# Kernel tuning notes

Measured on AMD Instinct MI355X. Metric: run time of the kernel, lower is better.

## Reference

```python
import jax, jax.numpy as jnp
import numpy as np

D_IN = 1024
D_OUT = 1024
NUM_HEADS = 16
HEAD_DIM = D_OUT // NUM_HEADS


def setup_inputs() -> dict:
    key = jax.random.key(0)
    kx, kq, kk, kv = jax.random.split(key, 4)
    x = jax.random.normal(kx, (2, 2048, D_IN), dtype=jnp.float32)
    W_q = jax.random.normal(kq, (D_IN, D_OUT), dtype=jnp.float32)
    W_k = jax.random.normal(kk, (D_IN, D_OUT), dtype=jnp.float32)
    W_v = jax.random.normal(kv, (D_IN, D_OUT), dtype=jnp.float32)
    return {"x": x, "W_q": W_q, "W_k": W_k, "W_v": W_v}


def reference(x, W_q, W_k, W_v):
    B, S, _ = x.shape
    H, Dh = NUM_HEADS, HEAD_DIM
    # project and split heads -> [B, H, S, Dh]
    q = (x @ W_q).reshape(B, S, H, Dh).transpose(0, 2, 1, 3)
    k = (x @ W_k).reshape(B, S, H, Dh).transpose(0, 2, 1, 3)
    v = (x @ W_v).reshape(B, S, H, Dh).transpose(0, 2, 1, 3)
    scores = jnp.einsum('bhqd,bhkd->bhqk', q, k) / jnp.sqrt(jnp.float32(Dh))
    causal = jnp.tril(jnp.ones((S, S), dtype=bool))  # True where allowed
    scores = jnp.where(causal[None, None], scores, -jnp.inf)
    weights = jax.nn.softmax(scores, axis=-1)
    ctx = jnp.einsum('bhqk,bhkd->bhqd', weights, v)
    return ctx.transpose(0, 2, 1, 3).reshape(B, S, H * Dh)
```

## Files before the change

### kernel.cpp

```cpp
#include <hip/hip_runtime.h>
#include <hip/hip_bf16.h>

#define B 2
#define S 2048
#define DIN 1024
#define DOUT 1024
#define NH 16
#define DH 64
#define M_TOT (B * S)

typedef __attribute__((ext_vector_type(8))) short bf16x8;
typedef __attribute__((ext_vector_type(8))) unsigned short u16x8;
typedef __attribute__((ext_vector_type(4))) float f32x4;
typedef __attribute__((ext_vector_type(16))) float f32x16;

#define ASTRIDE 4194304
#define WSTRIDE 1048576

__device__ __forceinline__ ushort f2bf(float x) {
    union { float f; unsigned u; } c; c.f = x;
    unsigned r = (c.u + 0x7FFFu + ((c.u >> 16) & 1u)) >> 16;
    return (ushort)r;
}
__device__ __forceinline__ float bf2f(ushort h) {
    union { unsigned u; float f; } c; c.u = ((unsigned)h) << 16;
    return c.f;
}
__device__ __forceinline__ f32x4 mfma16(bf16x8 a, bf16x8 b, f32x4 c) {
    return __builtin_amdgcn_mfma_f32_16x16x32_bf16(a, b, c, 0, 0, 0);
}
__device__ __forceinline__ f32x16 mfma32(bf16x8 a, bf16x8 b, f32x16 c) {
    return __builtin_amdgcn_mfma_f32_32x32x16_bf16(a, b, c, 0, 0, 0);
}
__device__ __forceinline__ unsigned cvt_pk(float lo, float hi) {
    unsigned r;
    asm("v_cvt_pk_bf16_f32 %0, %1, %2" : "=v"(r) : "v"(lo), "v"(hi));
    return r;
}
__device__ __forceinline__ float exp2fast(float x) {
    float r;
    asm("v_exp_f32 %0, %1" : "=v"(r) : "v"(x));
    return r;
}


__global__ __launch_bounds__(256) void split_x(const float* __restrict__ x,
                                               ushort* __restrict__ xs) {
    const size_t gid = (size_t)blockIdx.x * 256 + threadIdx.x;
    const float4 v = *reinterpret_cast<const float4*>(x + gid * 4);
    const float in[4] = {v.x, v.y, v.z, v.w};
    ushort h0[4], h1[4];
#pragma unroll
    for (int e = 0; e < 4; ++e) {
        h0[e] = f2bf(in[e]);
        h1[e] = f2bf(in[e] - bf2f(h0[e]));
    }
    const size_t o = gid * 4;
    *reinterpret_cast<ushort4*>(xs + o)           = ushort4{h0[0], h0[1], h0[2], h0[3]};
    *reinterpret_cast<ushort4*>(xs + ASTRIDE + o) = ushort4{h1[0], h1[1], h1[2], h1[3]};
}

__global__ __launch_bounds__(256) void split_wT3(const float* __restrict__ W0,
                                                 const float* __restrict__ W1,
                                                 const float* __restrict__ W2,
                                                 ushort* __restrict__ wt) {
    __shared__ float Ws[64][68];
    const int tid = threadIdx.x;
    const int k0 = blockIdx.x << 6;
    const int n0 = blockIdx.y << 6;
    const int wi = blockIdx.z;
    const float* W = (wi == 0) ? W0 : (wi == 1) ? W1 : W2;
    ushort* wto = wt + (size_t)wi * 2 * WSTRIDE;

    const int r = tid >> 2;
    const int cb = (tid & 3) << 2;
#pragma unroll
    for (int it = 0; it < 4; ++it) {
        const int c = cb + (it << 4);
        *reinterpret_cast<float4*>(&Ws[r][c]) =
            *reinterpret_cast<const float4*>(&W[(size_t)(k0 + r) * 1024 + n0 + c]);
    }
    __syncthreads();
    const int rn = tid >> 2;
    const int kc = (tid & 3) << 4;
    u16x8 o0[2], o1[2];
#pragma unroll
    for (int half = 0; half < 2; ++half)
#pragma unroll
        for (int i = 0; i < 8; ++i) {
            const float x = Ws[kc + (half << 3) + i][rn];
            const ushort a = f2bf(x);
            o0[half][i] = a;
            o1[half][i] = f2bf(x - bf2f(a));
        }
    const size_t base = (size_t)(n0 + rn) * 1024 + k0 + kc;
    *reinterpret_cast<u16x8*>(wto + base)               = o0[0];
    *reinterpret_cast<u16x8*>(wto + base + 8)           = o0[1];
    *reinterpret_cast<u16x8*>(wto + WSTRIDE + base)     = o1[0];
    *reinterpret_cast<u16x8*>(wto + WSTRIDE + base + 8) = o1[1];
}

__global__ __launch_bounds__(256, 2) void proj_fused3(const ushort* __restrict__ xsp,
                                                      const ushort* __restrict__ wtsp,
                                                      float* __restrict__ qf,
                                                      ushort* __restrict__ ksp,
                                                      ushort* __restrict__ vtsp) {
    __shared__ __align__(16) ushort SL[36864];

    const int tid = threadIdx.x;
    const int lane = tid & 63;
    const int w = tid >> 6;
    const int swz = (blockIdx.x & 7) * 64 + (blockIdx.x >> 3);
    const int n0 = (swz & 15) << 6;
    const int m0 = (swz >> 4) << 7;
    const int col = lane & 15;
    const int glane = lane >> 4;
    const int lrow = lane >> 3;
    const int sl8 = ((lane & 7) ^ lrow) << 3;

    f32x4 accq[2][4], acck[2][4], accv[2][4];
#pragma unroll
    for (int mi = 0; mi < 2; ++mi)
#pragma unroll
        for (int nj = 0; nj < 4; ++nj) {
            accq[mi][nj] = f32x4{0.f, 0.f, 0.f, 0.f};
            acck[mi][nj] = f32x4{0.f, 0.f, 0.f, 0.f};
            accv[mi][nj] = f32x4{0.f, 0.f, 0.f, 0.f};
        }

    for (int k0 = 0; k0 < DIN; k0 += 64) {
        __syncthreads();
#pragma unroll
        for (int i = 0; i < 18; ++i) {
            const int u = (i << 2) | w;
            const ushort* g;
            if (u < 32) {
                const int sp = u >> 4, rb = u & 15;
                g = xsp + (size_t)sp * ASTRIDE + (size_t)(m0 + (rb << 3) + lrow) * 1024 + k0 + sl8;
            } else {
                const int v = u - 32;
                const int bi = v >> 3;
                const int rb = v & 7;
                g = wtsp + (size_t)bi * WSTRIDE + (size_t)(n0 + (rb << 3) + lrow) * 1024 + k0 + sl8;
            }
            __builtin_amdgcn_global_load_lds(g, &SL[u * 512], 16, 0, 0);
        }
        __syncthreads();

#pragma unroll
        for (int st = 0; st < 2; ++st) {
            const int sw = (((st << 2) | glane) ^ (col & 7)) << 3;
            bf16x8 a[2][2];
#pragma unroll
            for (int sp = 0; sp < 2; ++sp)
#pragma unroll
                for (int mi = 0; mi < 2; ++mi) {
                    const int arow = (w << 5) + (mi << 4) + col;
                    a[sp][mi] = *reinterpret_cast<const bf16x8*>(&SL[sp * 8192 + arow * 64 + sw]);
                }
#pragma unroll
            for (int nj = 0; nj < 4; ++nj) {
                const int brow = (nj << 4) + col;
                const int bb = 16384 + brow * 64 + sw;
                const bf16x8 bq0 = *reinterpret_cast<const bf16x8*>(&SL[bb]);
                const bf16x8 bq1 = *reinterpret_cast<const bf16x8*>(&SL[bb + 4096]);
                const bf16x8 bk0 = *reinterpret_cast<const bf16x8*>(&SL[bb + 8192]);
                const bf16x8 bk1 = *reinterpret_cast<const bf16x8*>(&SL[bb + 12288]);
                const bf16x8 bv0 = *reinterpret_cast<const bf16x8*>(&SL[bb + 16384]);
#pragma unroll
                for (int mi = 0; mi < 2; ++mi) {
                    accq[mi][nj] = mfma16(a[0][mi], bq0, accq[mi][nj]);
                    accq[mi][nj] = mfma16(a[1][mi], bq0, accq[mi][nj]);
                    accq[mi][nj] = mfma16(a[0][mi], bq1, accq[mi][nj]);
                    accq[mi][nj] = mfma16(a[1][mi], bq1, accq[mi][nj]);
                    acck[mi][nj] = mfma16(a[0][mi], bk0, acck[mi][nj]);
                    acck[mi][nj] = mfma16(a[1][mi], bk0, acck[mi][nj]);
                    acck[mi][nj] = mfma16(a[0][mi], bk1, acck[mi][nj]);
                    acck[mi][nj] = mfma16(a[1][mi], bk1, acck[mi][nj]);
                    accv[mi][nj] = mfma16(a[0][mi], bv0, accv[mi][nj]);
                    accv[mi][nj] = mfma16(a[1][mi], bv0, accv[mi][nj]);
                }
            }
        }
    }

    const int b = m0 >> 11;
    const int h = n0 >> 6;
    const size_t bh_off = (size_t)(b * NH + h) * S * DH;
#pragma unroll
    for (int mi = 0; mi < 2; ++mi)
#pragma unroll
        for (int r = 0; r < 4; ++r) {
            const int srow = (m0 & (S - 1)) + (w << 5) + (mi << 4) + (glane << 2) + r;
#pragma unroll
            for (int nj = 0; nj < 4; ++nj) {
                const size_t o = bh_off + (size_t)srow * DH + (nj << 4) + col;
                qf[o] = accq[mi][nj][r];
                const float xk = acck[mi][nj][r];
                const ushort k0s = f2bf(xk);
                ksp[o] = k0s;
                ksp[ASTRIDE + o] = f2bf(xk - bf2f(k0s));
            }
        }

    float* SLf = reinterpret_cast<float*>(SL);
    __syncthreads();
#pragma unroll
    for (int mi = 0; mi < 2; ++mi)
#pragma unroll
        for (int r = 0; r < 4; ++r) {
            const int sl_ = (w << 5) + (mi << 4) + (glane << 2) + r;
#pragma unroll
            for (int nj = 0; nj < 4; ++nj)
                SLf[((nj << 4) + col) * 132 + sl_] = accv[mi][nj][r];
        }
    __syncthreads();
    {
        const int d = tid >> 2;
        const size_t vb = ((size_t)(b * NH + h) * DH + d) * S + (m0 & (S - 1));
#pragma unroll
        for (int blk = 0; blk < 2; ++blk) {
            const int sb = ((tid & 3) << 5) + (blk << 4);
            u16x8 oA, oB;
#pragma unroll
            for (int i = 0; i < 8; ++i) {
                const int jA = (i < 4) ? i : i + 4;
                const int jB = (i < 4) ? i + 4 : i + 8;
                oA[i] = f2bf(SLf[d * 132 + sb + jA]);
                oB[i] = f2bf(SLf[d * 132 + sb + jB]);
            }
            *reinterpret_cast<u16x8*>(vtsp + vb + sb)     = oA;
            *reinterpret_cast<u16x8*>(vtsp + vb + sb + 8) = oB;
        }
    }
}

__global__ __launch_bounds__(256, 2) void attn_mfma7(const float* __restrict__ Qf,
                                                     const ushort* __restrict__ ksp,
                                                     const ushort* __restrict__ vtsp,
                                                     float* __restrict__ out) {
    __shared__ __align__(16) ushort SB[2][12288];

    const int tid = threadIdx.x;
    const int lane = tid & 63;
    const int w = tid >> 6;

    const int xcd = blockIdx.x & 7;
    const int u_ = blockIdx.x >> 3;
    int bh, qt;
    if (u_ < 32) { bh = (xcd << 2) | (u_ >> 4);                 qt = 15 - (u_ & 15); }
    else         { const int v2 = u_ - 32; bh = (xcd << 2) | 2 | (v2 >> 4); qt = v2 & 15; }

    const int q0 = qt << 7;
    const int qw0 = q0 + (w << 5);
    const int hi = lane >> 5;
    const int ql = lane & 31;
    const int qg = qw0 + ql;
    const int lrow = lane >> 3;
    const int sl8 = ((lane & 7) ^ lrow) << 3;

    bf16x8 qb[3][4];
    {
        const float* qp = Qf + ((size_t)bh * S + qg) * DH + (hi << 3);
#pragma unroll
        for (int dc = 0; dc < 4; ++dc) {
            const float4 f0 = *reinterpret_cast<const float4*>(qp + (dc << 4));
            const float4 f1 = *reinterpret_cast<const float4*>(qp + (dc << 4) + 4);
            const float xs[8] = {f0.x, f0.y, f0.z, f0.w, f1.x, f1.y, f1.z, f1.w};
#pragma unroll
            for (int e = 0; e < 8; ++e) {
                const float x = xs[e] * 0.18033688011112042f;
                const ushort h0 = f2bf(x);
                const float r1 = x - bf2f(h0);
                const ushort h1 = f2bf(r1);
                qb[0][dc][e] = (short)h0;
                qb[1][dc][e] = (short)h1;
                qb[2][dc][e] = (short)f2bf(r1 - bf2f(h1));
            }
        }
    }

    f32x16 O[2];
#pragma unroll
    for (int ds = 0; ds < 2; ++ds)
#pragma unroll
        for (int r = 0; r < 16; ++r) O[ds][r] = 0.f;
    float m_ = -INFINITY, l_ = 0.f;

    const size_t kbase = (size_t)bh * S * DH;
    const size_t vbase = (size_t)bh * DH * S;

#define ISSUE_KV(K0, BUF)                                                               \
    {                                                                                   \
        _Pragma("unroll")                                                               \
        for (int i = 0; i < 6; ++i) {                                                   \
            const int u = (i << 2) | w;                                                 \
            const ushort* gp;                                                           \
            if (u < 16) {                                                               \
                const int sp = u >> 3, rb = u & 7;                                      \
                gp = ksp + (size_t)sp * ASTRIDE + kbase +                               \
                     (size_t)((K0) + (rb << 3) + lrow) * DH + sl8;                      \
            } else {                                                                    \
                const int rb = u & 7;                                                   \
                gp = vtsp + vbase + (size_t)((rb << 3) + lrow) * S + (K0) + sl8;        \
            }                                                                           \
            __builtin_amdgcn_global_load_lds(gp, &SB[BUF][u * 512], 16, 0, 0);          \
        }                                                                               \
    }

    ISSUE_KV(0, 0);
    __syncthreads();

    const int ktmax = (q0 >> 6) + 1;
    for (int kt = 0; kt <= ktmax; ++kt) {
        const int k0 = kt << 6;
        const int cur = kt & 1;
        if (kt < ktmax) ISSUE_KV(k0 + 64, cur ^ 1);

        const bool active = (k0 <= qw0 + 31);
        if (active) {
            const ushort* KL = &SB[cur][0];
            const ushort* VL = &SB[cur][8192];

            f32x16 Sf[2];
#pragma unroll
            for (int ks = 0; ks < 2; ++ks)
#pragma unroll
                for (int r = 0; r < 16; ++r) Sf[ks][r] = 0.f;
#pragma unroll
            for (int ks = 0; ks < 2; ++ks) {
#pragma unroll
                for (int dc = 0; dc < 4; ++dc) {
                    const int row = (ks << 5) + ql;
                    const int eo = row * 64 + ((((dc << 1) | hi) ^ (row & 7)) << 3);
                    const bf16x8 ka = *reinterpret_cast<const bf16x8*>(&KL[eo]);
                    const bf16x8 kb = *reinterpret_cast<const bf16x8*>(&KL[4096 + eo]);
                    Sf[ks] = mfma32(ka, qb[0][dc], Sf[ks]);
                    Sf[ks] = mfma32(ka, qb[1][dc], Sf[ks]);
                    Sf[ks] = mfma32(ka, qb[2][dc], Sf[ks]);
                    Sf[ks] = mfma32(kb, qb[0][dc], Sf[ks]);
                    Sf[ks] = mfma32(kb, qb[1][dc], Sf[ks]);
                }
            }

            if (k0 + 63 > qw0) {
#pragma unroll
                for (int ks = 0; ks < 2; ++ks)
#pragma unroll
                    for (int r = 0; r < 16; ++r) {
                        const int kg = k0 + (ks << 5) + (r & 3) + ((r >> 2) << 3) + (hi << 2);
                        if (kg > qg) Sf[ks][r] = -1e30f;
                    }
            }

            float mx[8];
#pragma unroll
            for (int i = 0; i < 8; ++i)
                mx[i] = fmaxf(fmaxf(Sf[0][i], Sf[0][i + 8]),
                              fmaxf(Sf[1][i], Sf[1][i + 8]));
            float rm = fmaxf(fmaxf(fmaxf(mx[0], mx[1]), fmaxf(mx[2], mx[3])),
                             fmaxf(fmaxf(mx[4], mx[5]), fmaxf(mx[6], mx[7])));
            rm = fmaxf(rm, __shfl_xor(rm, 32));
            if (__any(rm > m_ + 8.f)) {
                const float nm = fmaxf(m_, rm);
                const float sc = exp2fast(m_ - nm);
                m_ = nm;
                l_ *= sc;
#pragma unroll
                for (int ds = 0; ds < 2; ++ds)
#pragma unroll
                    for (int r = 0; r < 16; ++r) O[ds][r] *= sc;
            }

            float rsa[4] = {0.f, 0.f, 0.f, 0.f};
            bf16x8 pb[4];
#pragma unroll
            for (int ks = 0; ks < 2; ++ks) {
                float p[16];
#pragma unroll
                for (int r = 0; r < 16; ++r) {
                    p[r] = exp2fast(Sf[ks][r] - m_);
                    rsa[r & 3] += p[r];
                }
#pragma unroll
                for (int c = 0; c < 2; ++c) {
                    union { unsigned u[4]; bf16x8 v; } pw;
                    pw.u[0] = cvt_pk(p[(c << 3) + 0], p[(c << 3) + 1]);
                    pw.u[1] = cvt_pk(p[(c << 3) + 2], p[(c << 3) + 3]);
                    pw.u[2] = cvt_pk(p[(c << 3) + 4], p[(c << 3) + 5]);
                    pw.u[3] = cvt_pk(p[(c << 3) + 6], p[(c << 3) + 7]);
                    pb[(ks << 1) + c] = pw.v;
                }
            }
            float rs = (rsa[0] + rsa[1]) + (rsa[2] + rsa[3]);
            rs += __shfl_xor(rs, 32);
            l_ += rs;

#pragma unroll
            for (int ds = 0; ds < 2; ++ds)
#pragma unroll
                for (int kc = 0; kc < 4; ++kc) {
                    const int row = (ds << 5) + ql;
                    const int eo = row * 64 + ((((kc << 1) | hi) ^ (row & 7)) << 3);
                    const bf16x8 va = *reinterpret_cast<const bf16x8*>(&VL[eo]);
                    O[ds] = mfma32(va, pb[kc], O[ds]);
                }
        }
        __syncthreads();
    }

    const float inv = 1.f / l_;
    const int b = bh >> 4, h = bh & (NH - 1);
    float* op = out + ((size_t)(b * S + qg)) * DOUT + h * DH;
#pragma unroll
    for (int ds = 0; ds < 2; ++ds)
#pragma unroll
        for (int rg = 0; rg < 4; ++rg) {
            float4 v;
            v.x = O[ds][(rg << 2) + 0] * inv;
            v.y = O[ds][(rg << 2) + 1] * inv;
            v.z = O[ds][(rg << 2) + 2] * inv;
            v.w = O[ds][(rg << 2) + 3] * inv;
            *reinterpret_cast<float4*>(&op[(ds << 5) + (rg << 3) + (hi << 2)]) = v;
        }
#undef ISSUE_KV
}

__global__ __launch_bounds__(256) void proj_f32(const float* __restrict__ A,
                                                const float* __restrict__ W,
                                                float* __restrict__ outf) {
    __shared__ float As[16][68];
    __shared__ float Bs[16][68];
    const int tid = threadIdx.x;
    const int m0 = blockIdx.x * 64;
    const int n0 = blockIdx.y * 64;
    const int tm = tid >> 4, tn = tid & 15;
    const int la_r = tid >> 2, la_c = (tid & 3) << 2;
    const int lb_r = tid >> 4, lb_c = (tid & 15) << 2;

    float acc[4][4];
#pragma unroll
    for (int i = 0; i < 4; ++i)
#pragma unroll
        for (int j = 0; j < 4; ++j) acc[i][j] = 0.f;

    for (int k0 = 0; k0 < DIN; k0 += 16) {
        const float4 av = *reinterpret_cast<const float4*>(&A[(size_t)(m0 + la_r) * DIN + k0 + la_c]);
        const float4 bv = *reinterpret_cast<const float4*>(&W[(size_t)(k0 + lb_r) * DOUT + n0 + lb_c]);
        __syncthreads();
        As[la_c + 0][la_r] = av.x; As[la_c + 1][la_r] = av.y;
        As[la_c + 2][la_r] = av.z; As[la_c + 3][la_r] = av.w;
        *reinterpret_cast<float4*>(&Bs[lb_r][lb_c]) = bv;
        __syncthreads();
#pragma unroll
        for (int kk = 0; kk < 16; ++kk) {
            const float4 a = *reinterpret_cast<const float4*>(&As[kk][tm << 2]);
            const float4 b = *reinterpret_cast<const float4*>(&Bs[kk][tn << 2]);
            const float aa[4] = {a.x, a.y, a.z, a.w};
            const float bb[4] = {b.x, b.y, b.z, b.w};
#pragma unroll
            for (int i = 0; i < 4; ++i)
#pragma unroll
                for (int j = 0; j < 4; ++j) acc[i][j] += aa[i] * bb[j];
        }
    }
    const int b = m0 >> 11;
    const int s_base = (m0 & (S - 1)) + (tm << 2);
    const int h = n0 >> 6;
    const int dh = tn << 2;
    float* obase = outf + ((size_t)(b * NH + h) * S) * DH;
#pragma unroll
    for (int i = 0; i < 4; ++i) {
        float4 v;
        v.x = acc[i][0]; v.y = acc[i][1]; v.z = acc[i][2]; v.w = acc[i][3];
        *reinterpret_cast<float4*>(&obase[(size_t)(s_base + i) * DH + dh]) = v;
    }
}

__global__ __launch_bounds__(256) void attn_f32(const float* __restrict__ Q,
                                                const float* __restrict__ K,
                                                const float* __restrict__ V,
                                                float* __restrict__ out) {
    __shared__ float Qs[64][68];
    __shared__ float Ks[64][68];
    __shared__ float Vs[64][68];
    __shared__ float Ps[64][68];
    const int tid = threadIdx.x;
    const int bh = blockIdx.x & 31;
    const int qt = 31 - (blockIdx.x >> 5);
    const int q0 = qt << 6;
    const int tq = tid >> 4, tk = tid & 15;
    const int sr = tid >> 2, sc = (tid & 3) << 2;

    const float* qbase = Q + ((size_t)bh * S + q0) * DH;
    const float* kbase = K + (size_t)bh * S * DH;
    const float* vbase = V + (size_t)bh * S * DH;
#pragma unroll
    for (int it = 0; it < 4; ++it) {
        const int d0 = sc + (it << 4);
        const float4 v = *reinterpret_cast<const float4*>(&qbase[(size_t)sr * DH + d0]);
        Qs[d0 + 0][sr] = v.x; Qs[d0 + 1][sr] = v.y;
        Qs[d0 + 2][sr] = v.z; Qs[d0 + 3][sr] = v.w;
    }
    float C[4][4];
#pragma unroll
    for (int i = 0; i < 4; ++i)
#pragma unroll
        for (int j = 0; j < 4; ++j) C[i][j] = 0.f;
    float m[4] = {-1e30f, -1e30f, -1e30f, -1e30f};
    float l[4] = {0.f, 0.f, 0.f, 0.f};

    for (int kt = 0; kt <= qt; ++kt) {
        const int k0 = kt << 6;
        float4 kv[4], vv[4];
#pragma unroll
        for (int it = 0; it < 4; ++it) {
            const int d0 = sc + (it << 4);
            kv[it] = *reinterpret_cast<const float4*>(&kbase[(size_t)(k0 + sr) * DH + d0]);
            vv[it] = *reinterpret_cast<const float4*>(&vbase[(size_t)(k0 + sr) * DH + d0]);
        }
        __syncthreads();
#pragma unroll
        for (int it = 0; it < 4; ++it) {
            const int d0 = sc + (it << 4);
            Ks[d0 + 0][sr] = kv[it].x; Ks[d0 + 1][sr] = kv[it].y;
            Ks[d0 + 2][sr] = kv[it].z; Ks[d0 + 3][sr] = kv[it].w;
            *reinterpret_cast<float4*>(&Vs[sr][d0]) = vv[it];
        }
        __syncthreads();

        float s[4][4];
#pragma unroll
        for (int i = 0; i < 4; ++i)
#pragma unroll
            for (int j = 0; j < 4; ++j) s[i][j] = 0.f;
#pragma unroll 16
        for (int d = 0; d < 64; ++d) {
            const float4 qf4 = *reinterpret_cast<const float4*>(&Qs[d][tq << 2]);
            const float4 kf4 = *reinterpret_cast<const float4*>(&Ks[d][tk << 2]);
            const float qa[4] = {qf4.x, qf4.y, qf4.z, qf4.w};
            const float ka[4] = {kf4.x, kf4.y, kf4.z, kf4.w};
#pragma unroll
            for (int i = 0; i < 4; ++i)
#pragma unroll
                for (int j = 0; j < 4; ++j) s[i][j] += qa[i] * ka[j];
        }
        if (kt == qt) {
#pragma unroll
            for (int i = 0; i < 4; ++i) {
                const int qg = q0 + (tq << 2) + i;
#pragma unroll
                for (int j = 0; j < 4; ++j) {
                    const int kg = k0 + (tk << 2) + j;
                    s[i][j] = (kg <= qg) ? s[i][j] * 0.125f : -1e30f;
                }
            }
        } else {
#pragma unroll
            for (int i = 0; i < 4; ++i)
#pragma unroll
                for (int j = 0; j < 4; ++j) s[i][j] *= 0.125f;
        }
#pragma unroll
        for (int i = 0; i < 4; ++i) {
            float rm = fmaxf(fmaxf(s[i][0], s[i][1]), fmaxf(s[i][2], s[i][3]));
#pragma unroll
            for (int off = 1; off < 16; off <<= 1) rm = fmaxf(rm, __shfl_xor(rm, off));
            const float mn = fmaxf(m[i], rm);
            const float scale = __expf(m[i] - mn);
            float rs = 0.f;
#pragma unroll
            for (int j = 0; j < 4; ++j) {
                s[i][j] = __expf(s[i][j] - mn);
                rs += s[i][j];
            }
#pragma unroll
            for (int off = 1; off < 16; off <<= 1) rs += __shfl_xor(rs, off);
            l[i] = l[i] * scale + rs;
            m[i] = mn;
#pragma unroll
            for (int j = 0; j < 4; ++j) C[i][j] *= scale;
            *reinterpret_cast<float4*>(&Ps[(tq << 2) + i][tk << 2]) =
                make_float4(s[i][0], s[i][1], s[i][2], s[i][3]);
        }
        __syncthreads();
#pragma unroll 4
        for (int kc = 0; kc < 16; ++kc) {
            float4 pf[4], vf[4];
#pragma unroll
            for (int i = 0; i < 4; ++i)
                pf[i] = *reinterpret_cast<const float4*>(&Ps[(tq << 2) + i][kc << 2]);
#pragma unroll
            for (int j = 0; j < 4; ++j)
                vf[j] = *reinterpret_cast<const float4*>(&Vs[(kc << 2) + j][tk << 2]);
#pragma unroll
            for (int i = 0; i < 4; ++i) {
                const float pa[4] = {pf[i].x, pf[i].y, pf[i].z, pf[i].w};
#pragma unroll
                for (int j = 0; j < 4; ++j) {
                    C[i][j] += pa[0] * ((const float*)&vf[0])[j]
                             + pa[1] * ((const float*)&vf[1])[j]
                             + pa[2] * ((const float*)&vf[2])[j]
                             + pa[3] * ((const float*)&vf[3])[j];
                }
            }
        }
        __syncthreads();
    }
    const int b = bh >> 4, h = bh & (NH - 1);
#pragma unroll
    for (int i = 0; i < 4; ++i) {
        const int qg = q0 + (tq << 2) + i;
        const float inv = 1.f / l[i];
        float4 v;
        v.x = C[i][0] * inv; v.y = C[i][1] * inv;
        v.z = C[i][2] * inv; v.w = C[i][3] * inv;
        *reinterpret_cast<float4*>(&out[((size_t)(b * S + qg)) * DOUT + h * DH + (tk << 2)]) = v;
    }
}

extern "C" void kernel_launch(void* const* d_in, const int* in_sizes, int n_in,
                              void* d_out, int out_size, void* d_ws, size_t ws_size,
                              hipStream_t stream) {
    const float* x  = (const float*)d_in[0];
    const float* Wq = (const float*)d_in[1];
    const float* Wk = (const float*)d_in[2];
    const float* Wv = (const float*)d_in[3];
    float* out = (float*)d_out;

    char* ws = (char*)d_ws;
    const size_t MB = 1024 * 1024;

    if (ws_size >= 68 * MB) {
        ushort* wtsp = (ushort*)(ws);
        ushort* xsp  = (ushort*)(ws + 12 * MB);
        float*  qf   = (float*)(ws + 28 * MB);
        ushort* ksp  = (ushort*)(ws + 44 * MB);
        ushort* vtsp = (ushort*)(ws + 60 * MB);

        split_x<<<4096, 256, 0, stream>>>(x, xsp);
        split_wT3<<<dim3(16, 16, 3), 256, 0, stream>>>(Wq, Wk, Wv, wtsp);
        proj_fused3<<<512, 256, 0, stream>>>(xsp, wtsp, qf, ksp, vtsp);
        attn_mfma7<<<512, 256, 0, stream>>>(qf, ksp, vtsp, out);
    } else {
        float* qws = (float*)d_ws;
        float* kws = qws + (size_t)M_TOT * DOUT;
        float* vws = kws + (size_t)M_TOT * DOUT;
        dim3 pgrid(M_TOT / 64, DOUT / 64);
        proj_f32<<<pgrid, 256, 0, stream>>>(x, Wq, qws);
        proj_f32<<<pgrid, 256, 0, stream>>>(x, Wk, kws);
        proj_f32<<<pgrid, 256, 0, stream>>>(x, Wv, vws);
        attn_f32<<<32 * 32, 256, 0, stream>>>(qws, kws, vws, out);
    }
}
```

Before: 144.5 us.

## Double-buffer projection LDS tiles, drop lo*lo MFMA terms, transpose V via MFMA operand swap

The fused QKV projection now double-buffers its shared-memory tiles, issuing the next K-slice's global-to-LDS loads before computing on the current one, so each step needs one barrier instead of two. It also drops the lo*lo correction MFMAs in the split-bf16 products, which lowers precision slightly. V is computed with swapped MFMA operands so the accumulator comes out already transposed and is stored directly, removing the LDS transpose pass. LDS use doubles to about 144KB per block, which may cut occupancy from two blocks per CU to one.

```diff
diff --git a/kernel.cpp b/kernel.cpp
--- a/kernel.cpp
+++ b/kernel.cpp
@@ -100,12 +100,12 @@
     *reinterpret_cast<u16x8*>(wto + WSTRIDE + base + 8) = o1[1];
 }
 
-__global__ __launch_bounds__(256, 2) void proj_fused3(const ushort* __restrict__ xsp,
-                                                      const ushort* __restrict__ wtsp,
-                                                      float* __restrict__ qf,
-                                                      ushort* __restrict__ ksp,
-                                                      ushort* __restrict__ vtsp) {
-    __shared__ __align__(16) ushort SL[36864];
+__global__ __launch_bounds__(256) void proj_fused4(const ushort* __restrict__ xsp,
+                                                   const ushort* __restrict__ wtsp,
+                                                   float* __restrict__ qf,
+                                                   ushort* __restrict__ ksp,
+                                                   ushort* __restrict__ vtsp) {
+    __shared__ __align__(16) ushort SB[2][36864];
 
     const int tid = threadIdx.x;
     const int lane = tid & 63;
@@ -128,25 +128,35 @@
             accv[mi][nj] = f32x4{0.f, 0.f, 0.f, 0.f};
         }
 
-    for (int k0 = 0; k0 < DIN; k0 += 64) {
-        __syncthreads();
-#pragma unroll
-        for (int i = 0; i < 18; ++i) {
-            const int u = (i << 2) | w;
-            const ushort* g;
-            if (u < 32) {
-                const int sp = u >> 4, rb = u & 15;
-                g = xsp + (size_t)sp * ASTRIDE + (size_t)(m0 + (rb << 3) + lrow) * 1024 + k0 + sl8;
-            } else {
-                const int v = u - 32;
-                const int bi = v >> 3;
-                const int rb = v & 7;
-                g = wtsp + (size_t)bi * WSTRIDE + (size_t)(n0 + (rb << 3) + lrow) * 1024 + k0 + sl8;
-            }
-            __builtin_amdgcn_global_load_lds(g, &SL[u * 512], 16, 0, 0);
-        }
-        __syncthreads();
-
+#define PISSUE(K0, BUF)                                                                 \
+    {                                                                                   \
+        _Pragma("unroll")                                                               \
+        for (int i = 0; i < 18; ++i) {                                                  \
+            const int u = (i << 2) | w;                                                 \
+            const ushort* g;                                                            \
+            if (u < 32) {                                                               \
+                const int sp = u >> 4, rb = u & 15;                                     \
+                g = xsp + (size_t)sp * ASTRIDE +                                        \
+                    (size_t)(m0 + (rb << 3) + lrow) * 1024 + (K0) + sl8;                \
+            } else {                                                                    \
+                const int v = u - 32;                                                   \
+                const int bi = v >> 3;                  \
+                const int rb = v & 7;                                                   \
+                g = wtsp + (size_t)bi * WSTRIDE +                                       \
+                    (size_t)(n0 + (rb << 3) + lrow) * 1024 + (K0) + sl8;                \
+            }                                                                           \
+            __builtin_amdgcn_global_load_lds(g, &SB[BUF][u * 512], 16, 0, 0);           \
+        }                                                                               \
+    }
+
+    PISSUE(0, 0);
+    __syncthreads();
+
+    for (int kt = 0; kt < 16; ++kt) {
+        const int cur = kt & 1;
+        if (kt < 15) PISSUE((kt + 1) << 6, cur ^ 1);
+
+        const ushort* SL = SB[cur];
 #pragma unroll
         for (int st = 0; st < 2; ++st) {
             const int sw = (((st << 2) | glane) ^ (col & 7)) << 3;
@@ -172,17 +182,17 @@
                     accq[mi][nj] = mfma16(a[0][mi], bq0, accq[mi][nj]);
                     accq[mi][nj] = mfma16(a[1][mi], bq0, accq[mi][nj]);
                     accq[mi][nj] = mfma16(a[0][mi], bq1, accq[mi][nj]);
-                    accq[mi][nj] = mfma16(a[1][mi], bq1, accq[mi][nj]);
                     acck[mi][nj] = mfma16(a[0][mi], bk0, acck[mi][nj]);
                     acck[mi][nj] = mfma16(a[1][mi], bk0, acck[mi][nj]);
                     acck[mi][nj] = mfma16(a[0][mi], bk1, acck[mi][nj]);
-                    acck[mi][nj] = mfma16(a[1][mi], bk1, acck[mi][nj]);
-                    accv[mi][nj] = mfma16(a[0][mi], bv0, accv[mi][nj]);
-                    accv[mi][nj] = mfma16(a[1][mi], bv0, accv[mi][nj]);
-                }
-            }
-        }
-    }
+                    accv[mi][nj] = mfma16(bv0, a[0][mi], accv[mi][nj]);
+                    accv[mi][nj] = mfma16(bv0, a[1][mi], accv[mi][nj]);
+                }
+            }
+        }
+        __syncthreads();
+    }
+#undef PISSUE
 
     const int b = m0 >> 11;
     const int h = n0 >> 6;
@@ -203,35 +213,19 @@
             }
         }
 
-    float* SLf = reinterpret_cast<float*>(SL);
-    __syncthreads();
-#pragma unroll
-    for (int mi = 0; mi < 2; ++mi)
-#pragma unroll
-        for (int r = 0; r < 4; ++r) {
-            const int sl_ = (w << 5) + (mi << 4) + (glane << 2) + r;
-#pragma unroll
-            for (int nj = 0; nj < 4; ++nj)
-                SLf[((nj << 4) + col) * 132 + sl_] = accv[mi][nj][r];
-        }
-    __syncthreads();
-    {
-        const int d = tid >> 2;
-        const size_t vb = ((size_t)(b * NH + h) * DH + d) * S + (m0 & (S - 1));
-#pragma unroll
-        for (int blk = 0; blk < 2; ++blk) {
-            const int sb = ((tid & 3) << 5) + (blk << 4);
-            u16x8 oA, oB;
-#pragma unroll
-            for (int i = 0; i < 8; ++i) {
-                const int jA = (i < 4) ? i : i + 4;
-                const int jB = (i < 4) ? i + 4 : i + 8;
-                oA[i] = f2bf(SLf[d * 132 + sb + jA]);
-                oB[i] = f2bf(SLf[d * 132 + sb + jB]);
-            }
-            *reinterpret_cast<u16x8*>(vtsp + vb + sb)     = oA;
-            *reinterpret_cast<u16x8*>(vtsp + vb + sb + 8) = oB;
-        }
+    const int cm = col >> 2;
+    const int colp = (col & 3) | ((((cm & 1) << 1) | (cm >> 1)) << 2);
+    const size_t vbh = (size_t)(b * NH + h) * DH * S;
+#pragma unroll
+    for (int mi = 0; mi < 2; ++mi) {
+        const int s = (m0 & (S - 1)) + (w << 5) + (mi << 4) + colp;
+#pragma unroll
+        for (int nj = 0; nj < 4; ++nj)
+#pragma unroll
+            for (int r = 0; r < 4; ++r) {
+                const int d = (nj << 4) + (glane << 2) + r;
+                vtsp[vbh + (size_t)d * S + s] = f2bf(accv[mi][nj][r]);
+            }
     }
 }
 
@@ -640,7 +634,7 @@
 
         split_x<<<4096, 256, 0, stream>>>(x, xsp);
         split_wT3<<<dim3(16, 16, 3), 256, 0, stream>>>(Wq, Wk, Wv, wtsp);
-        proj_fused3<<<512, 256, 0, stream>>>(xsp, wtsp, qf, ksp, vtsp);
+        proj_fused4<<<512, 256, 0, stream>>>(xsp, wtsp, qf, ksp, vtsp);
         attn_mfma7<<<512, 256, 0, stream>>>(qf, ksp, vtsp, out);
     } else {
         float* qws = (float*)d_ws;
```

Measured after the change: 143.4 us. No clear change (-0.7%).

## Drop lo*lo split-bf16 MFMAs and write V transposed directly from registers

Applied to the files above, without the earlier changes.

Removes the lo×lo correction MFMA from the Q and K split-bf16 products, cutting one of four MFMAs per term. V now uses hi×hi plus lo-x×hi-W only. The V MFMA operands are swapped so the accumulator comes out transposed, which lets V^T be stored straight from registers with a permuted column index. That replaces the shared-memory transpose and its two barriers. The trade is a small loss of precision and narrower, less coalesced 2-byte scattered stores for V^T.

```diff
diff --git a/kernel.cpp b/kernel.cpp
--- a/kernel.cpp
+++ b/kernel.cpp
@@ -100,7 +100,7 @@
     *reinterpret_cast<u16x8*>(wto + WSTRIDE + base + 8) = o1[1];
 }
 
-__global__ __launch_bounds__(256, 2) void proj_fused3(const ushort* __restrict__ xsp,
+__global__ __launch_bounds__(256, 2) void proj_fused5(const ushort* __restrict__ xsp,
                                                       const ushort* __restrict__ wtsp,
                                                       float* __restrict__ qf,
                                                       ushort* __restrict__ ksp,
@@ -172,13 +172,11 @@
                     accq[mi][nj] = mfma16(a[0][mi], bq0, accq[mi][nj]);
                     accq[mi][nj] = mfma16(a[1][mi], bq0, accq[mi][nj]);
                     accq[mi][nj] = mfma16(a[0][mi], bq1, accq[mi][nj]);
-                    accq[mi][nj] = mfma16(a[1][mi], bq1, accq[mi][nj]);
                     acck[mi][nj] = mfma16(a[0][mi], bk0, acck[mi][nj]);
                     acck[mi][nj] = mfma16(a[1][mi], bk0, acck[mi][nj]);
                     acck[mi][nj] = mfma16(a[0][mi], bk1, acck[mi][nj]);
-                    acck[mi][nj] = mfma16(a[1][mi], bk1, acck[mi][nj]);
-                    accv[mi][nj] = mfma16(a[0][mi], bv0, accv[mi][nj]);
-                    accv[mi][nj] = mfma16(a[1][mi], bv0, accv[mi][nj]);
+                    accv[mi][nj] = mfma16(bv0, a[0][mi], accv[mi][nj]);
+                    accv[mi][nj] = mfma16(bv0, a[1][mi], accv[mi][nj]);
                 }
             }
         }
@@ -203,35 +201,19 @@
             }
         }
 
-    float* SLf = reinterpret_cast<float*>(SL);
-    __syncthreads();
-#pragma unroll
-    for (int mi = 0; mi < 2; ++mi)
-#pragma unroll
-        for (int r = 0; r < 4; ++r) {
-            const int sl_ = (w << 5) + (mi << 4) + (glane << 2) + r;
-#pragma unroll
-            for (int nj = 0; nj < 4; ++nj)
-                SLf[((nj << 4) + col) * 132 + sl_] = accv[mi][nj][r];
-        }
-    __syncthreads();
-    {
-        const int d = tid >> 2;
-        const size_t vb = ((size_t)(b * NH + h) * DH + d) * S + (m0 & (S - 1));
-#pragma unroll
-        for (int blk = 0; blk < 2; ++blk) {
-            const int sb = ((tid & 3) << 5) + (blk << 4);
-            u16x8 oA, oB;
-#pragma unroll
-            for (int i = 0; i < 8; ++i) {
-                const int jA = (i < 4) ? i : i + 4;
-                const int jB = (i < 4) ? i + 4 : i + 8;
-                oA[i] = f2bf(SLf[d * 132 + sb + jA]);
-                oB[i] = f2bf(SLf[d * 132 + sb + jB]);
-            }
-            *reinterpret_cast<u16x8*>(vtsp + vb + sb)     = oA;
-            *reinterpret_cast<u16x8*>(vtsp + vb + sb + 8) = oB;
-        }
+    const int cm = col >> 2;
+    const int colp = (col & 3) | ((((cm & 1) << 1) | (cm >> 1)) << 2);
+    const size_t vbh = (size_t)(b * NH + h) * DH * S;
+#pragma unroll
+    for (int mi = 0; mi < 2; ++mi) {
+        const int s = (m0 & (S - 1)) + (w << 5) + (mi << 4) + colp;
+#pragma unroll
+        for (int nj = 0; nj < 4; ++nj)
+#pragma unroll
+            for (int r = 0; r < 4; ++r) {
+                const int d = (nj << 4) + (glane << 2) + r;
+                vtsp[vbh + (size_t)d * S + s] = f2bf(accv[mi][nj][r]);
+            }
     }
 }
 
@@ -640,7 +622,7 @@
 
         split_x<<<4096, 256, 0, stream>>>(x, xsp);
         split_wT3<<<dim3(16, 16, 3), 256, 0, stream>>>(Wq, Wk, Wv, wtsp);
-        proj_fused3<<<512, 256, 0, stream>>>(xsp, wtsp, qf, ksp, vtsp);
+        proj_fused5<<<512, 256, 0, stream>>>(xsp, wtsp, qf, ksp, vtsp);
         attn_mfma7<<<512, 256, 0, stream>>>(qf, ksp, vtsp, out);
     } else {
         float* qws = (float*)d_ws;
```

Result: faster. 133.4 us (-7.7%).
